# Optimization experiments

Hardware: AMD Instinct MI355X
Metric: run time of the kernel (lower is better)

## Reference

```python
import jax, jax.numpy as jnp
import numpy as np

B, T, H, V = 32, 256, 1024, 50257


def setup_inputs() -> dict:
    key = jax.random.key(0)
    k1, k2, k3, k4 = jax.random.split(key, 4)
    # log-normalized HMM parameters, matching torch.log_softmax in __init__
    alpha = jax.nn.log_softmax(jax.random.normal(k1, (H, H), dtype=jnp.float32), axis=1)
    beta = jax.nn.log_softmax(jax.random.normal(k2, (H, V), dtype=jnp.float32), axis=1)
    gamma = jax.nn.log_softmax(jax.random.normal(k3, (H,), dtype=jnp.float32), axis=0)
    x = jax.random.randint(k4, (B, T), 0, V)
    return {"x": x, "alpha": alpha, "beta": beta, "gamma": gamma}


def reference(x, alpha, beta, gamma):
    # emission log-probs gathered per token: e[b, t, h] = beta[h, x[b, t]]
    e = beta.T[x]  # [B, T, H]

    # backward-in-time recurrence:
    #   y_{T-1} = e[:, T-1]
    #   y_t     = logsumexp_j(alpha[i, j] + y_{t+1}[b, j]) + e[:, t]
    y0 = e[:, -1]  # [B, H]

    def step(y, e_t):
        y = jax.nn.logsumexp(alpha[None, :, :] + y[:, None, :], axis=2) + e_t
        return y, None

    # scan over t = T-2 .. 0 (reverse time order)
    es = jnp.flip(e[:, :-1], axis=1).transpose(1, 0, 2)  # [T-1, B, H]
    y, _ = jax.lax.scan(step, y0, es)

    # final marginalization over initial-state distribution gamma
    return jax.nn.logsumexp(gamma[None, :] + y, axis=1)  # [B]
```

## Files before the change

### kernel.cpp

```cpp
#include <hip/hip_runtime.h>
#include <hip/hip_bf16.h>


#define Hdim 1024
#define Bdim 32
#define Tdim 256
#define Vdim 50257
#define NWG  16
#define SLICE 64

typedef __attribute__((ext_vector_type(8))) __bf16 bf16x8;
typedef __attribute__((ext_vector_type(4))) float  f32x4;
typedef __attribute__((ext_vector_type(4))) unsigned u32x4;

#define OFF_ABF   0
#define OFF_YBUF  2097152
#define OFF_PSUM  (OFF_YBUF + 131072)
#define OFF_RBUF  (OFF_PSUM + 128)
#define OFF_WREC  (OFF_RBUF + 128)
#define OFF_FLG   (OFF_WREC + 8192)
#define OFF_END0  (OFF_FLG + 8192)
#define OFF_E     (((OFF_END0) + 4095) & ~4095)
#define WS_E_NEED ((size_t)OFF_E + (size_t)Tdim * Bdim * Hdim * 4)

#define SM_A       131072
#define SMEM_BYTES (SM_A + 256)

__device__ __forceinline__ void st_b128_sc(void* p, u32x4 v) {
    asm volatile("global_store_dwordx4 %0, %1, off sc0 sc1" :: "v"(p), "v"(v) : "memory");
}
__device__ __forceinline__ void st_b32_sc(void* p, unsigned v) {
    asm volatile("global_store_dword %0, %1, off sc0 sc1" :: "v"(p), "v"(v) : "memory");
}
__device__ __forceinline__ void st_b16_sc(void* p, unsigned v) {
    asm volatile("global_store_short %0, %1, off sc0 sc1" :: "v"(p), "v"(v) : "memory");
}
__device__ __forceinline__ u32x4 ld_b128_sc(const void* p) {
    u32x4 r;
    asm volatile("global_load_dwordx4 %0, %1, off sc0 sc1" : "=v"(r) : "v"(p) : "memory");
    return r;
}
__device__ __forceinline__ float ld_f32_sc(const void* p) {
    float r;
    asm volatile("global_load_dword %0, %1, off sc0 sc1" : "=v"(r) : "v"(p) : "memory");
    return r;
}
__device__ __forceinline__ unsigned ld_u32sync_sc(const void* p) {
    unsigned r;
    asm volatile("global_load_dword %0, %1, off sc0 sc1\n\ts_waitcnt vmcnt(0)"
                 : "=v"(r) : "v"(p) : "memory");
    return r;
}
__device__ __forceinline__ void waitcnt_vm0() {
    asm volatile("s_waitcnt vmcnt(0)" ::: "memory");
    __builtin_amdgcn_sched_barrier(0);
}
__device__ __forceinline__ void waitcnt_vm32() {
    asm volatile("s_waitcnt vmcnt(32)" ::: "memory");
    __builtin_amdgcn_sched_barrier(0);
}

__global__ void k_expA(const float* __restrict__ alpha, __bf16* __restrict__ Abf) {
    int idx = (blockIdx.x * 256 + threadIdx.x) * 4;
    float4 v = *(const float4*)(alpha + idx);
    union { __bf16 h[4]; uint2 u; } cv;
    cv.h[0] = (__bf16)__expf(v.x);
    cv.h[1] = (__bf16)__expf(v.y);
    cv.h[2] = (__bf16)__expf(v.z);
    cv.h[3] = (__bf16)__expf(v.w);
    *(uint2*)(Abf + idx) = cv.u;
}

__global__ void k_gather(const int* __restrict__ x, const float* __restrict__ beta,
                         float* __restrict__ E) {
    int tb = blockIdx.x;
    int t  = tb >> 5, b = tb & 31;
    int xv = x[b * Tdim + t];
    int i  = threadIdx.x * 4;
    float4 v;
    v.x = beta[(size_t)(i + 0) * Vdim + xv];
    v.y = beta[(size_t)(i + 1) * Vdim + xv];
    v.z = beta[(size_t)(i + 2) * Vdim + xv];
    v.w = beta[(size_t)(i + 3) * Vdim + xv];
    *(float4*)(E + ((size_t)t * Bdim + b) * Hdim + i) = v;
}

__device__ __forceinline__ void load_e(const float* __restrict__ E,
                                       const float* __restrict__ beta,
                                       const int* __restrict__ x,
                                       int t, int b0, int i0, int useE, float e[2][4]) {
    if (useE) {
        #pragma unroll
        for (int u = 0; u < 2; ++u)
            #pragma unroll
            for (int r = 0; r < 4; ++r)
                e[u][r] = E[((size_t)t * Bdim + (b0 + r)) * Hdim + i0 + u * 16];
    } else {
        int xv[4];
        #pragma unroll
        for (int r = 0; r < 4; ++r) xv[r] = x[(b0 + r) * Tdim + t];
        #pragma unroll
        for (int u = 0; u < 2; ++u)
            #pragma unroll
            for (int r = 0; r < 4; ++r)
                e[u][r] = beta[(size_t)(i0 + u * 16) * Vdim + xv[r]];
    }
}

__device__ __forceinline__ void publish_wave(const float y[2][4], const float Gc[4],
                                             char* Yblk,
                                             char* wrec_pw,
                                             char* flg_pw,
                                             int li, int g, int np, int b0,
                                             unsigned seq) {
    float mx[4];
    #pragma unroll
    for (int r = 0; r < 4; ++r) {
        #pragma unroll
        for (int u = 0; u < 2; ++u) {
            float Yn = __expf(y[u][r] - Gc[r]);
            __bf16 h = (__bf16)Yn;
            unsigned hv = (unsigned)__builtin_bit_cast(unsigned short, h);
            st_b16_sc(Yblk + (b0 + r) * 128 + (np * 32 + u * 16 + li) * 2, hv);
        }
        float m = fmaxf(y[0][r], y[1][r]);
        m = fmaxf(m, __shfl_xor(m, 1, 16));
        m = fmaxf(m, __shfl_xor(m, 2, 16));
        m = fmaxf(m, __shfl_xor(m, 4, 16));
        m = fmaxf(m, __shfl_xor(m, 8, 16));
        mx[r] = m;
    }
    if (li == 0) {
        f32x4 mv = {mx[0], mx[1], mx[2], mx[3]};
        st_b128_sc(wrec_pw + g * 16, __builtin_bit_cast(u32x4, mv));
    }
    asm volatile("s_waitcnt vmcnt(0)" ::: "memory");
    if ((threadIdx.x & 63) == 0) st_b32_sc(flg_pw, seq);
}

__launch_bounds__(256, 1)
__global__ void k_hmm(const int* __restrict__ x,
                      const float* __restrict__ beta,
                      const float* __restrict__ gamma,
                      const __bf16* __restrict__ Abf,
                      char* __restrict__ Yb,
                      char* __restrict__ wrec,
                      char* __restrict__ flg,
                      float* __restrict__ Psum,
                      float* __restrict__ Rbuf,
                      const float* __restrict__ Ebuf,
                      int useE)
{
    extern __shared__ char smem[];
    char* Asl = smem;

    const int p   = blockIdx.x;
    const int tid = threadIdx.x;
    const int w   = tid >> 6;
    const int l   = tid & 63;
    const int g   = l >> 4;
    const int li  = l & 15;
    const int mb  = w & 1;
    const int np  = w >> 1;
    const int b0  = mb * 16 + g * 4;
    const int i0  = p * SLICE + np * 32 + li;

    #pragma unroll
    for (int rep = 0; rep < 32; ++rep) {
        int flat = rep * 256 + tid;
        int row  = flat >> 7;
        int c16  = flat & 127;
        uint4 v = *(const uint4*)((const char*)Abf + (size_t)(p * 64 + row) * 2048 + c16 * 16);
        int off = (row * 2048 + c16 * 16) ^ ((row & 7) << 4);
        *(uint4*)(Asl + off) = v;
    }
    __syncthreads();

    {
        float y0[2][4];
        load_e(Ebuf, beta, x, Tdim - 1, b0, i0, useE, y0);
        float Gc0[4] = {0.f, 0.f, 0.f, 0.f};
        publish_wave(y0, Gc0, Yb + p * 4096,
                     wrec + (size_t)p * 256 + w * 64,
                     flg + (size_t)(p * 4 + w) * 64,
                     li, g, np, b0, 1u);
    }

    float Nprev[4] = {0.f, 0.f, 0.f, 0.f};
    float ereg[2][4];
    load_e(Ebuf, beta, x, Tdim - 2, b0, i0, useE, ereg);

    for (int s = 1; s < Tdim; ++s) {
        const int t     = Tdim - 1 - s;
        const int par_r = (s - 1) & 1;
        const int par_w = s & 1;

        float eregN[2][4];
        if (s < Tdim - 1) load_e(Ebuf, beta, x, t - 1, b0, i0, useE, eregN);
        float gl[2] = {0.f, 0.f};
        if (s == Tdim - 1) { gl[0] = gamma[i0]; gl[1] = gamma[i0 + 16]; }
        waitcnt_vm0();

        {
            const char* fp = flg + (size_t)par_r * 4096 + l * 64;
            while (!__all((int)(ld_u32sync_sc(fp) >= (unsigned)s))) {}
        }

        const char* Ybase = Yb + (size_t)par_r * (NWG * 4096);
        const char* yrow  = Ybase + (mb * 16 + li) * 128 + g * 16;
        u32x4 yreg[32];
        #pragma unroll
        for (int kc = 0; kc < 32; ++kc)
            yreg[kc] = ld_b128_sc(yrow + (kc >> 1) * 4096 + (kc & 1) * 64);

        float gmv[32];
        {
            const char* wbase = wrec + (size_t)par_r * 4096;
            if (l < 32) {
                int bmb = l >> 4;
                int idx = (l & 15) * 4;
                #pragma unroll
                for (int q = 0; q < 16; ++q) {
                    gmv[2 * q]     = ld_f32_sc(wbase + q * 256 + bmb * 64 + idx);
                    gmv[2 * q + 1] = ld_f32_sc(wbase + q * 256 + (bmb + 2) * 64 + idx);
                }
            }
        }

        waitcnt_vm32();

        f32x4 acc0 = {0.f, 0.f, 0.f, 0.f}, acc1 = {0.f, 0.f, 0.f, 0.f};
        {
            const int ia = np * 32 + li;
            const int ib = ia + 16;
            const int basea = ia * 2048 + g * 16, xa = (ia & 7) << 4;
            const int baseb = ib * 2048 + g * 16, xb = (ib & 7) << 4;
            #pragma unroll
            for (int kc = 0; kc < 32; ++kc) {
                bf16x8 af0 = *(const bf16x8*)(Asl + ((basea + kc * 64) ^ xa));
                bf16x8 af1 = *(const bf16x8*)(Asl + ((baseb + kc * 64) ^ xb));
                bf16x8 yf  = __builtin_bit_cast(bf16x8, yreg[kc]);
                acc0 = __builtin_amdgcn_mfma_f32_16x16x32_bf16(yf, af0, acc0, 0, 0, 0);
                acc1 = __builtin_amdgcn_mfma_f32_16x16x32_bf16(yf, af1, acc1, 0, 0, 0);
            }
        }

        waitcnt_vm0();

        float gm = -3.0e38f;
        if (l < 32) {
            #pragma unroll
            for (int q = 0; q < 32; ++q) gm = fmaxf(gm, gmv[q]);
        }
        float Gcur[4];
        #pragma unroll
        for (int r = 0; r < 4; ++r) Gcur[r] = __shfl(gm, b0 + r);

        float yv[2][4];
        #pragma unroll
        for (int r = 0; r < 4; ++r) {
            yv[0][r] = Nprev[r] + __logf(acc0[r]) + ereg[0][r];
            yv[1][r] = Nprev[r] + __logf(acc1[r]) + ereg[1][r];
        }

        if (s < Tdim - 1) {
            publish_wave(yv, Gcur,
                         Yb + (size_t)par_w * (NWG * 4096) + p * 4096,
                         wrec + (size_t)par_w * 4096 + (size_t)p * 256 + w * 64,
                         flg + (size_t)par_w * 4096 + (size_t)(p * 4 + w) * 64,
                         li, g, np, b0, (unsigned)(s + 1));
            #pragma unroll
            for (int r = 0; r < 4; ++r) Nprev[r] = Gcur[r];
            #pragma unroll
            for (int u = 0; u < 2; ++u)
                #pragma unroll
                for (int r = 0; r < 4; ++r) ereg[u][r] = eregN[u][r];
        } else {
            #pragma unroll
            for (int r = 0; r < 4; ++r) {
                float pa = __expf(gl[0] + yv[0][r] - Gcur[r])
                         + __expf(gl[1] + yv[1][r] - Gcur[r]);
                pa += __shfl_xor(pa, 1, 16);
                pa += __shfl_xor(pa, 2, 16);
                pa += __shfl_xor(pa, 4, 16);
                pa += __shfl_xor(pa, 8, 16);
                if (li == 0) {
                    atomicAdd(&Psum[b0 + r], pa);
                    if (p == 0) Rbuf[b0 + r] = Gcur[r];
                }
            }
        }
    }
}

__global__ void k_final(const float* __restrict__ Psum, const float* __restrict__ Rbuf,
                        float* __restrict__ out) {
    int b = threadIdx.x;
    if (b < 32) out[b] = Rbuf[b] + __logf(Psum[b]);
}

extern "C" void kernel_launch(void* const* d_in, const int* in_sizes, int n_in,
                              void* d_out, int out_size, void* d_ws, size_t ws_size,
                              hipStream_t stream) {
    const int*   x     = (const int*)d_in[0];
    const float* alpha = (const float*)d_in[1];
    const float* beta  = (const float*)d_in[2];
    const float* gamma = (const float*)d_in[3];

    char* ws = (char*)d_ws;
    __bf16* Abf  = (__bf16*)(ws + OFF_ABF);
    char*   Yb   = ws + OFF_YBUF;
    float*  Psum = (float*)(ws + OFF_PSUM);
    float*  Rbuf = (float*)(ws + OFF_RBUF);
    char*   wrec = ws + OFF_WREC;
    char*   flg  = ws + OFF_FLG;
    float*  Ebuf = (float*)(ws + OFF_E);

    int useE = (ws_size >= WS_E_NEED) ? 1 : 0;

    (void)hipMemsetAsync(ws + OFF_PSUM, 0, OFF_END0 - OFF_PSUM, stream);

    hipLaunchKernelGGL(k_expA, dim3((Hdim * Hdim) / (256 * 4)), dim3(256), 0, stream, alpha, Abf);

    if (useE)
        hipLaunchKernelGGL(k_gather, dim3(Tdim * Bdim), dim3(256), 0, stream, x, beta, Ebuf);

    (void)hipFuncSetAttribute((const void*)k_hmm, hipFuncAttributeMaxDynamicSharedMemorySize, SMEM_BYTES);
    hipLaunchKernelGGL(k_hmm, dim3(NWG), dim3(256), SMEM_BYTES, stream,
                       x, beta, gamma, Abf, Yb, wrec, flg, Psum, Rbuf,
                       useE ? Ebuf : (const float*)nullptr, useE);

    hipLaunchKernelGGL(k_final, dim3(1), dim3(64), 0, stream, Psum, Rbuf, (float*)d_out);
}
```

Baseline: 2.018 ms.

## Replace flag-based grid sync with sign-tagged data validity polling

Removes the separate per-wave flag stores and the flag spin-wait. Consumers now repeatedly load the Y buffer and the max records until every value carries the expected epoch tag. The tag is the bf16 sign bit, which flips every two steps via a negation factor, and the max records are paired with a step tag. Each step then needs one store-to-load round trip instead of two (data wait, then flag), at the cost of re-reading the full Y tile on every failed poll. The Y buffer is pre-filled so the initial sign pattern matches no valid epoch.

```diff
diff --git a/kernel.cpp b/kernel.cpp
--- a/kernel.cpp
+++ b/kernel.cpp
@@ -12,51 +12,38 @@
 typedef __attribute__((ext_vector_type(8))) __bf16 bf16x8;
 typedef __attribute__((ext_vector_type(4))) float  f32x4;
 typedef __attribute__((ext_vector_type(4))) unsigned u32x4;
+typedef __attribute__((ext_vector_type(2))) unsigned u32x2;
 
 #define OFF_ABF   0
 #define OFF_YBUF  2097152
 #define OFF_PSUM  (OFF_YBUF + 131072)
 #define OFF_RBUF  (OFF_PSUM + 128)
 #define OFF_WREC  (OFF_RBUF + 128)
-#define OFF_FLG   (OFF_WREC + 8192)
-#define OFF_END0  (OFF_FLG + 8192)
+#define OFF_END0  (OFF_WREC + 16384)
 #define OFF_E     (((OFF_END0) + 4095) & ~4095)
 #define WS_E_NEED ((size_t)OFF_E + (size_t)Tdim * Bdim * Hdim * 4)
 
 #define SM_A       131072
 #define SMEM_BYTES (SM_A + 256)
 
-__device__ __forceinline__ void st_b128_sc(void* p, u32x4 v) {
-    asm volatile("global_store_dwordx4 %0, %1, off sc0 sc1" :: "v"(p), "v"(v) : "memory");
-}
-__device__ __forceinline__ void st_b32_sc(void* p, unsigned v) {
-    asm volatile("global_store_dword %0, %1, off sc0 sc1" :: "v"(p), "v"(v) : "memory");
-}
 __device__ __forceinline__ void st_b16_sc(void* p, unsigned v) {
     asm volatile("global_store_short %0, %1, off sc0 sc1" :: "v"(p), "v"(v) : "memory");
+}
+__device__ __forceinline__ void st_b64_sc(void* p, u32x2 v) {
+    asm volatile("global_store_dwordx2 %0, %1, off sc0 sc1" :: "v"(p), "v"(v) : "memory");
 }
 __device__ __forceinline__ u32x4 ld_b128_sc(const void* p) {
     u32x4 r;
     asm volatile("global_load_dwordx4 %0, %1, off sc0 sc1" : "=v"(r) : "v"(p) : "memory");
     return r;
 }
-__device__ __forceinline__ float ld_f32_sc(const void* p) {
-    float r;
-    asm volatile("global_load_dword %0, %1, off sc0 sc1" : "=v"(r) : "v"(p) : "memory");
-    return r;
-}
-__device__ __forceinline__ unsigned ld_u32sync_sc(const void* p) {
-    unsigned r;
-    asm volatile("global_load_dword %0, %1, off sc0 sc1\n\ts_waitcnt vmcnt(0)"
-                 : "=v"(r) : "v"(p) : "memory");
+__device__ __forceinline__ u32x2 ld_b64_sc(const void* p) {
+    u32x2 r;
+    asm volatile("global_load_dwordx2 %0, %1, off sc0 sc1" : "=v"(r) : "v"(p) : "memory");
     return r;
 }
 __device__ __forceinline__ void waitcnt_vm0() {
     asm volatile("s_waitcnt vmcnt(0)" ::: "memory");
-    __builtin_amdgcn_sched_barrier(0);
-}
-__device__ __forceinline__ void waitcnt_vm32() {
-    asm volatile("s_waitcnt vmcnt(32)" ::: "memory");
     __builtin_amdgcn_sched_barrier(0);
 }
 
@@ -109,17 +96,16 @@
 
 __device__ __forceinline__ void publish_wave(const float y[2][4], const float Gc[4],
                                              char* Yblk,
-                                             char* wrec_pw,
-                                             char* flg_pw,
+                                             char* wrec_w,
                                              int li, int g, int np, int b0,
-                                             unsigned seq) {
+                                             unsigned tag, float wneg) {
     float mx[4];
     #pragma unroll
     for (int r = 0; r < 4; ++r) {
         #pragma unroll
         for (int u = 0; u < 2; ++u) {
             float Yn = __expf(y[u][r] - Gc[r]);
-            __bf16 h = (__bf16)Yn;
+            __bf16 h = (__bf16)(Yn * wneg);
             unsigned hv = (unsigned)__builtin_bit_cast(unsigned short, h);
             st_b16_sc(Yblk + (b0 + r) * 128 + (np * 32 + u * 16 + li) * 2, hv);
         }
@@ -131,11 +117,12 @@
         mx[r] = m;
     }
     if (li == 0) {
-        f32x4 mv = {mx[0], mx[1], mx[2], mx[3]};
-        st_b128_sc(wrec_pw + g * 16, __builtin_bit_cast(u32x4, mv));
-    }
-    asm volatile("s_waitcnt vmcnt(0)" ::: "memory");
-    if ((threadIdx.x & 63) == 0) st_b32_sc(flg_pw, seq);
+        #pragma unroll
+        for (int r = 0; r < 4; ++r) {
+            u32x2 pr = { __builtin_bit_cast(unsigned, mx[r]), tag };
+            st_b64_sc(wrec_w + g * 32 + r * 8, pr);
+        }
+    }
 }
 
 __launch_bounds__(256, 1)
@@ -145,7 +132,6 @@
                       const __bf16* __restrict__ Abf,
                       char* __restrict__ Yb,
                       char* __restrict__ wrec,
-                      char* __restrict__ flg,
                       float* __restrict__ Psum,
                       float* __restrict__ Rbuf,
                       const float* __restrict__ Ebuf,
@@ -165,6 +151,11 @@
     const int b0  = mb * 16 + g * 4;
     const int i0  = p * SLICE + np * 32 + li;
 
+    const int wl_bmb = (l >> 4) & 1;
+    const int wl_w   = wl_bmb + ((l >> 5) << 1);
+    const int wl_bi  = l & 15;
+    const int wl_off = wl_w * 128 + (wl_bi >> 2) * 32 + (wl_bi & 3) * 8;
+
     #pragma unroll
     for (int rep = 0; rep < 32; ++rep) {
         int flat = rep * 256 + tid;
@@ -181,9 +172,8 @@
         load_e(Ebuf, beta, x, Tdim - 1, b0, i0, useE, y0);
         float Gc0[4] = {0.f, 0.f, 0.f, 0.f};
         publish_wave(y0, Gc0, Yb + p * 4096,
-                     wrec + (size_t)p * 256 + w * 64,
-                     flg + (size_t)(p * 4 + w) * 64,
-                     li, g, np, b0, 1u);
+                     wrec + (size_t)p * 512 + w * 128,
+                     li, g, np, b0, 1u, 1.f);
     }
 
     float Nprev[4] = {0.f, 0.f, 0.f, 0.f};
@@ -194,40 +184,54 @@
         const int t     = Tdim - 1 - s;
         const int par_r = (s - 1) & 1;
         const int par_w = s & 1;
+        const unsigned want = (unsigned)s;
+        const unsigned sgnr = (((s - 1) >> 1) & 1) ? 0x80008000u : 0u;
+        const float    negr = (((s - 1) >> 1) & 1) ? -1.f : 1.f;
+        const float    negw = ((s >> 1) & 1) ? -1.f : 1.f;
 
         float eregN[2][4];
         if (s < Tdim - 1) load_e(Ebuf, beta, x, t - 1, b0, i0, useE, eregN);
         float gl[2] = {0.f, 0.f};
         if (s == Tdim - 1) { gl[0] = gamma[i0]; gl[1] = gamma[i0 + 16]; }
-        waitcnt_vm0();
-
-        {
-            const char* fp = flg + (size_t)par_r * 4096 + l * 64;
-            while (!__all((int)(ld_u32sync_sc(fp) >= (unsigned)s))) {}
-        }
 
         const char* Ybase = Yb + (size_t)par_r * (NWG * 4096);
         const char* yrow  = Ybase + (mb * 16 + li) * 128 + g * 16;
+        const char* wbase = wrec + (size_t)par_r * 8192 + wl_off;
+
         u32x4 yreg[32];
-        #pragma unroll
-        for (int kc = 0; kc < 32; ++kc)
-            yreg[kc] = ld_b128_sc(yrow + (kc >> 1) * 4096 + (kc & 1) * 64);
-
-        float gmv[32];
-        {
-            const char* wbase = wrec + (size_t)par_r * 4096;
-            if (l < 32) {
-                int bmb = l >> 4;
-                int idx = (l & 15) * 4;
-                #pragma unroll
-                for (int q = 0; q < 16; ++q) {
-                    gmv[2 * q]     = ld_f32_sc(wbase + q * 256 + bmb * 64 + idx);
-                    gmv[2 * q + 1] = ld_f32_sc(wbase + q * 256 + (bmb + 2) * 64 + idx);
-                }
+        u32x2 wr[16];
+        int okc;
+        do {
+            #pragma unroll
+            for (int kc = 0; kc < 32; ++kc)
+                yreg[kc] = ld_b128_sc(yrow + (kc >> 1) * 4096 + (kc & 1) * 64);
+            #pragma unroll
+            for (int q = 0; q < 16; ++q)
+                wr[q] = ld_b64_sc(wbase + q * 512);
+            waitcnt_vm0();
+            unsigned bad = 0;
+            #pragma unroll
+            for (int kc = 0; kc < 32; ++kc) {
+                bad |= (yreg[kc][0] ^ sgnr) & 0x80008000u;
+                bad |= (yreg[kc][1] ^ sgnr) & 0x80008000u;
+                bad |= (yreg[kc][2] ^ sgnr) & 0x80008000u;
+                bad |= (yreg[kc][3] ^ sgnr) & 0x80008000u;
             }
-        }
-
-        waitcnt_vm32();
+            #pragma unroll
+            for (int q = 0; q < 16; ++q)
+                bad |= (wr[q][1] ^ want);
+            okc = __all(bad == 0);
+        } while (!okc);
+
+        float gm = __builtin_bit_cast(float, wr[0][0]);
+        #pragma unroll
+        for (int q = 1; q < 16; ++q)
+            gm = fmaxf(gm, __builtin_bit_cast(float, wr[q][0]));
+        gm = fmaxf(gm, __shfl_xor(gm, 32));
+
+        float Gcur[4];
+        #pragma unroll
+        for (int r = 0; r < 4; ++r) Gcur[r] = __shfl(gm, mb * 16 + g * 4 + r);
 
         f32x4 acc0 = {0.f, 0.f, 0.f, 0.f}, acc1 = {0.f, 0.f, 0.f, 0.f};
         {
@@ -245,30 +249,18 @@
             }
         }
 
-        waitcnt_vm0();
-
-        float gm = -3.0e38f;
-        if (l < 32) {
-            #pragma unroll
-            for (int q = 0; q < 32; ++q) gm = fmaxf(gm, gmv[q]);
-        }
-        float Gcur[4];
-        #pragma unroll
-        for (int r = 0; r < 4; ++r) Gcur[r] = __shfl(gm, b0 + r);
-
         float yv[2][4];
         #pragma unroll
         for (int r = 0; r < 4; ++r) {
-            yv[0][r] = Nprev[r] + __logf(acc0[r]) + ereg[0][r];
-            yv[1][r] = Nprev[r] + __logf(acc1[r]) + ereg[1][r];
+            yv[0][r] = Nprev[r] + __logf(acc0[r] * negr) + ereg[0][r];
+            yv[1][r] = Nprev[r] + __logf(acc1[r] * negr) + ereg[1][r];
         }
 
         if (s < Tdim - 1) {
             publish_wave(yv, Gcur,
                          Yb + (size_t)par_w * (NWG * 4096) + p * 4096,
-                         wrec + (size_t)par_w * 4096 + (size_t)p * 256 + w * 64,
-                         flg + (size_t)par_w * 4096 + (size_t)(p * 4 + w) * 64,
-                         li, g, np, b0, (unsigned)(s + 1));
+                         wrec + (size_t)par_w * 8192 + (size_t)p * 512 + w * 128,
+                         li, g, np, b0, (unsigned)(s + 1), negw);
             #pragma unroll
             for (int r = 0; r < 4; ++r) Nprev[r] = Gcur[r];
             #pragma unroll
@@ -313,11 +305,11 @@
     float*  Psum = (float*)(ws + OFF_PSUM);
     float*  Rbuf = (float*)(ws + OFF_RBUF);
     char*   wrec = ws + OFF_WREC;
-    char*   flg  = ws + OFF_FLG;
     float*  Ebuf = (float*)(ws + OFF_E);
 
     int useE = (ws_size >= WS_E_NEED) ? 1 : 0;
 
+    (void)hipMemsetAsync(ws + OFF_YBUF, 0xAA, 131072, stream);
     (void)hipMemsetAsync(ws + OFF_PSUM, 0, OFF_END0 - OFF_PSUM, stream);
 
     hipLaunchKernelGGL(k_expA, dim3((Hdim * Hdim) / (256 * 4)), dim3(256), 0, stream, alpha, Abf);
@@ -327,7 +319,7 @@
 
     (void)hipFuncSetAttribute((const void*)k_hmm, hipFuncAttributeMaxDynamicSharedMemorySize, SMEM_BYTES);
     hipLaunchKernelGGL(k_hmm, dim3(NWG), dim3(256), SMEM_BYTES, stream,
-                       x, beta, gamma, Abf, Yb, wrec, flg, Psum, Rbuf,
+                       x, beta, gamma, Abf, Yb, wrec, Psum, Rbuf,
                        useE ? Ebuf : (const float*)nullptr, useE);
 
     hipLaunchKernelGGL(k_final, dim3(1), dim3(64), 0, stream, Psum, Rbuf, (float*)d_out);
```

Result: slower. 2.920 ms (+44.7%).

## Replace per-wave flag polling with atomic counters and overlap emission loads

Applied to the files above, without the earlier changes.

Each wave now publishes by atomically incrementing one shared per-parity counter, instead of writing its own sequence flag. Consumers spin on a single counter load rather than 64 flag loads combined with a wave-wide all-reduce. In the E-buffer path, the next step's emission loads are issued after the Y loads and use cached global loads, so they overlap with the MFMA work. A waitcnt of 8 keeps them outstanding. The kernel is templated on useE to drop the runtime branches, and the gamma load is hoisted out of the loop. The risk is contention on one atomic counter across 64 waves, plus the relaxed-ordering correctness of the counter handshake.

```diff
diff --git a/kernel.cpp b/kernel.cpp
--- a/kernel.cpp
+++ b/kernel.cpp
@@ -18,22 +18,23 @@
 #define OFF_PSUM  (OFF_YBUF + 131072)
 #define OFF_RBUF  (OFF_PSUM + 128)
 #define OFF_WREC  (OFF_RBUF + 128)
-#define OFF_FLG   (OFF_WREC + 8192)
-#define OFF_END0  (OFF_FLG + 8192)
+#define OFF_CNT   (OFF_WREC + 8192)
+#define OFF_END0  (OFF_CNT + 256)
 #define OFF_E     (((OFF_END0) + 4095) & ~4095)
 #define WS_E_NEED ((size_t)OFF_E + (size_t)Tdim * Bdim * Hdim * 4)
 
 #define SM_A       131072
 #define SMEM_BYTES (SM_A + 256)
 
+#define WAITCNT_VM(n) do { \
+    asm volatile("s_waitcnt vmcnt(" #n ")" ::: "memory"); \
+    __builtin_amdgcn_sched_barrier(0); } while (0)
+
+__device__ __forceinline__ void st_b16_sc(void* p, unsigned v) {
+    asm volatile("global_store_short %0, %1, off sc0 sc1" :: "v"(p), "v"(v) : "memory");
+}
 __device__ __forceinline__ void st_b128_sc(void* p, u32x4 v) {
     asm volatile("global_store_dwordx4 %0, %1, off sc0 sc1" :: "v"(p), "v"(v) : "memory");
-}
-__device__ __forceinline__ void st_b32_sc(void* p, unsigned v) {
-    asm volatile("global_store_dword %0, %1, off sc0 sc1" :: "v"(p), "v"(v) : "memory");
-}
-__device__ __forceinline__ void st_b16_sc(void* p, unsigned v) {
-    asm volatile("global_store_short %0, %1, off sc0 sc1" :: "v"(p), "v"(v) : "memory");
 }
 __device__ __forceinline__ u32x4 ld_b128_sc(const void* p) {
     u32x4 r;
@@ -45,19 +46,10 @@
     asm volatile("global_load_dword %0, %1, off sc0 sc1" : "=v"(r) : "v"(p) : "memory");
     return r;
 }
-__device__ __forceinline__ unsigned ld_u32sync_sc(const void* p) {
-    unsigned r;
-    asm volatile("global_load_dword %0, %1, off sc0 sc1\n\ts_waitcnt vmcnt(0)"
-                 : "=v"(r) : "v"(p) : "memory");
+__device__ __forceinline__ float ld_f32_cached(const void* p) {
+    float r;
+    asm volatile("global_load_dword %0, %1, off" : "=v"(r) : "v"(p) : "memory");
     return r;
-}
-__device__ __forceinline__ void waitcnt_vm0() {
-    asm volatile("s_waitcnt vmcnt(0)" ::: "memory");
-    __builtin_amdgcn_sched_barrier(0);
-}
-__device__ __forceinline__ void waitcnt_vm32() {
-    asm volatile("s_waitcnt vmcnt(32)" ::: "memory");
-    __builtin_amdgcn_sched_barrier(0);
 }
 
 __global__ void k_expA(const float* __restrict__ alpha, __bf16* __restrict__ Abf) {
@@ -110,9 +102,8 @@
 __device__ __forceinline__ void publish_wave(const float y[2][4], const float Gc[4],
                                              char* Yblk,
                                              char* wrec_pw,
-                                             char* flg_pw,
-                                             int li, int g, int np, int b0,
-                                             unsigned seq) {
+                                             unsigned* cnt_w,
+                                             int l, int li, int g, int np, int b0) {
     float mx[4];
     #pragma unroll
     for (int r = 0; r < 4; ++r) {
@@ -134,10 +125,12 @@
         f32x4 mv = {mx[0], mx[1], mx[2], mx[3]};
         st_b128_sc(wrec_pw + g * 16, __builtin_bit_cast(u32x4, mv));
     }
-    asm volatile("s_waitcnt vmcnt(0)" ::: "memory");
-    if ((threadIdx.x & 63) == 0) st_b32_sc(flg_pw, seq);
-}
-
+    WAITCNT_VM(0);
+    if (l == 0)
+        __hip_atomic_fetch_add(cnt_w, 1u, __ATOMIC_RELAXED, __HIP_MEMORY_SCOPE_AGENT);
+}
+
+template<int USEE>
 __launch_bounds__(256, 1)
 __global__ void k_hmm(const int* __restrict__ x,
                       const float* __restrict__ beta,
@@ -145,11 +138,10 @@
                       const __bf16* __restrict__ Abf,
                       char* __restrict__ Yb,
                       char* __restrict__ wrec,
-                      char* __restrict__ flg,
+                      unsigned* __restrict__ cnt,
                       float* __restrict__ Psum,
                       float* __restrict__ Rbuf,
-                      const float* __restrict__ Ebuf,
-                      int useE)
+                      const float* __restrict__ Ebuf)
 {
     extern __shared__ char smem[];
     char* Asl = smem;
@@ -176,34 +168,48 @@
     }
     __syncthreads();
 
+    const float gl0 = gamma[i0];
+    const float gl1 = gamma[i0 + 16];
+
     {
         float y0[2][4];
-        load_e(Ebuf, beta, x, Tdim - 1, b0, i0, useE, y0);
+        load_e(Ebuf, beta, x, Tdim - 1, b0, i0, USEE, y0);
         float Gc0[4] = {0.f, 0.f, 0.f, 0.f};
         publish_wave(y0, Gc0, Yb + p * 4096,
                      wrec + (size_t)p * 256 + w * 64,
-                     flg + (size_t)(p * 4 + w) * 64,
-                     li, g, np, b0, 1u);
+                     cnt, l, li, g, np, b0);
     }
 
     float Nprev[4] = {0.f, 0.f, 0.f, 0.f};
     float ereg[2][4];
-    load_e(Ebuf, beta, x, Tdim - 2, b0, i0, useE, ereg);
+    float eregN[2][4];
+
+    if constexpr (USEE) {
+        const float* Et = Ebuf + (size_t)(Tdim - 2) * (Bdim * Hdim);
+        #pragma unroll
+        for (int u = 0; u < 2; ++u)
+            #pragma unroll
+            for (int r = 0; r < 4; ++r)
+                ereg[u][r] = ld_f32_cached(Et + (b0 + r) * Hdim + i0 + u * 16);
+        WAITCNT_VM(0);
+    } else {
+        load_e(Ebuf, beta, x, Tdim - 2, b0, i0, 0, ereg);
+    }
 
     for (int s = 1; s < Tdim; ++s) {
         const int t     = Tdim - 1 - s;
         const int par_r = (s - 1) & 1;
         const int par_w = s & 1;
 
-        float eregN[2][4];
-        if (s < Tdim - 1) load_e(Ebuf, beta, x, t - 1, b0, i0, useE, eregN);
-        float gl[2] = {0.f, 0.f};
-        if (s == Tdim - 1) { gl[0] = gamma[i0]; gl[1] = gamma[i0 + 16]; }
-        waitcnt_vm0();
+        if constexpr (!USEE) {
+            if (s < Tdim - 1) load_e(Ebuf, beta, x, t - 1, b0, i0, 0, eregN);
+            WAITCNT_VM(0);
+        }
 
         {
-            const char* fp = flg + (size_t)par_r * 4096 + l * 64;
-            while (!__all((int)(ld_u32sync_sc(fp) >= (unsigned)s))) {}
+            const unsigned tgt = 64u * (((unsigned)s + 1u) >> 1);
+            unsigned* cp = cnt + (size_t)par_r * 32;
+            while (__hip_atomic_load(cp, __ATOMIC_RELAXED, __HIP_MEMORY_SCOPE_AGENT) < tgt) {}
         }
 
         const char* Ybase = Yb + (size_t)par_r * (NWG * 4096);
@@ -227,7 +233,18 @@
             }
         }
 
-        waitcnt_vm32();
+        if constexpr (USEE) {
+            const int tE = (t > 0) ? (t - 1) : 0;
+            const float* Et = Ebuf + (size_t)tE * (Bdim * Hdim);
+            #pragma unroll
+            for (int u = 0; u < 2; ++u)
+                #pragma unroll
+                for (int r = 0; r < 4; ++r)
+                    eregN[u][r] = ld_f32_cached(Et + (b0 + r) * Hdim + i0 + u * 16);
+            WAITCNT_VM(8);
+        } else {
+            WAITCNT_VM(0);
+        }
 
         f32x4 acc0 = {0.f, 0.f, 0.f, 0.f}, acc1 = {0.f, 0.f, 0.f, 0.f};
         {
@@ -245,8 +262,6 @@
             }
         }
 
-        waitcnt_vm0();
-
         float gm = -3.0e38f;
         if (l < 32) {
             #pragma unroll
@@ -267,8 +282,8 @@
             publish_wave(yv, Gcur,
                          Yb + (size_t)par_w * (NWG * 4096) + p * 4096,
                          wrec + (size_t)par_w * 4096 + (size_t)p * 256 + w * 64,
-                         flg + (size_t)par_w * 4096 + (size_t)(p * 4 + w) * 64,
-                         li, g, np, b0, (unsigned)(s + 1));
+                         cnt + (size_t)par_w * 32,
+                         l, li, g, np, b0);
             #pragma unroll
             for (int r = 0; r < 4; ++r) Nprev[r] = Gcur[r];
             #pragma unroll
@@ -278,8 +293,8 @@
         } else {
             #pragma unroll
             for (int r = 0; r < 4; ++r) {
-                float pa = __expf(gl[0] + yv[0][r] - Gcur[r])
-                         + __expf(gl[1] + yv[1][r] - Gcur[r]);
+                float pa = __expf(gl0 + yv[0][r] - Gcur[r])
+                         + __expf(gl1 + yv[1][r] - Gcur[r]);
                 pa += __shfl_xor(pa, 1, 16);
                 pa += __shfl_xor(pa, 2, 16);
                 pa += __shfl_xor(pa, 4, 16);
@@ -308,13 +323,13 @@
     const float* gamma = (const float*)d_in[3];
 
     char* ws = (char*)d_ws;
-    __bf16* Abf  = (__bf16*)(ws + OFF_ABF);
-    char*   Yb   = ws + OFF_YBUF;
-    float*  Psum = (float*)(ws + OFF_PSUM);
-    float*  Rbuf = (float*)(ws + OFF_RBUF);
-    char*   wrec = ws + OFF_WREC;
-    char*   flg  = ws + OFF_FLG;
-    float*  Ebuf = (float*)(ws + OFF_E);
+    __bf16*   Abf  = (__bf16*)(ws + OFF_ABF);
+    char*     Yb   = ws + OFF_YBUF;
+    float*    Psum = (float*)(ws + OFF_PSUM);
+    float*    Rbuf = (float*)(ws + OFF_RBUF);
+    char*     wrec = ws + OFF_WREC;
+    unsigned* cnt  = (unsigned*)(ws + OFF_CNT);
+    float*    Ebuf = (float*)(ws + OFF_E);
 
     int useE = (ws_size >= WS_E_NEED) ? 1 : 0;
 
@@ -322,13 +337,16 @@
 
     hipLaunchKernelGGL(k_expA, dim3((Hdim * Hdim) / (256 * 4)), dim3(256), 0, stream, alpha, Abf);
 
-    if (useE)
+    if (useE) {
         hipLaunchKernelGGL(k_gather, dim3(Tdim * Bdim), dim3(256), 0, stream, x, beta, Ebuf);
-
-    (void)hipFuncSetAttribute((const void*)k_hmm, hipFuncAttributeMaxDynamicSharedMemorySize, SMEM_BYTES);
-    hipLaunchKernelGGL(k_hmm, dim3(NWG), dim3(256), SMEM_BYTES, stream,
-                       x, beta, gamma, Abf, Yb, wrec, flg, Psum, Rbuf,
-                       useE ? Ebuf : (const float*)nullptr, useE);
+        (void)hipFuncSetAttribute((const void*)k_hmm<1>, hipFuncAttributeMaxDynamicSharedMemorySize, SMEM_BYTES);
+        hipLaunchKernelGGL(k_hmm<1>, dim3(NWG), dim3(256), SMEM_BYTES, stream,
+                           x, beta, gamma, Abf, Yb, wrec, cnt, Psum, Rbuf, Ebuf);
+    } else {
+        (void)hipFuncSetAttribute((const void*)k_hmm<0>, hipFuncAttributeMaxDynamicSharedMemorySize, SMEM_BYTES);
+        hipLaunchKernelGGL(k_hmm<0>, dim3(NWG), dim3(256), SMEM_BYTES, stream,
+                           x, beta, gamma, Abf, Yb, wrec, cnt, Psum, Rbuf, (const float*)nullptr);
+    }
 
     hipLaunchKernelGGL(k_final, dim3(1), dim3(64), 0, stream, Psum, Rbuf, (float*)d_out);
 }
```

Measured after the change: 2.341 ms. 16.0% more time.

## Fuse emission gather into recurrence kernel as extra blocks with per-timestep ready flags

Applied to the files above, without the earlier changes.

Removes the separate gather kernel. The gather work now runs as extra blocks of the recurrence launch, in reverse time order, so it overlaps with the sequential HMM recurrence. Each timestep's gather blocks bump an atomic ready counter, and recurrence blocks poll it before loading the emissions they need. Once a global counter shows all gathers are done, polling stops. The cost is polling latency inside the serial loop, and the gather blocks inherit the large dynamic LDS allocation, which may limit how many run concurrently.

```diff
diff --git a/kernel.cpp b/kernel.cpp
--- a/kernel.cpp
+++ b/kernel.cpp
@@ -8,6 +8,7 @@
 #define Vdim 50257
 #define NWG  16
 #define SLICE 64
+#define NGATHER (Tdim * Bdim)
 
 typedef __attribute__((ext_vector_type(8))) __bf16 bf16x8;
 typedef __attribute__((ext_vector_type(4))) float  f32x4;
@@ -19,21 +20,23 @@
 #define OFF_RBUF  (OFF_PSUM + 128)
 #define OFF_WREC  (OFF_RBUF + 128)
 #define OFF_FLG   (OFF_WREC + 8192)
-#define OFF_END0  (OFF_FLG + 8192)
+#define OFF_ERDY  (OFF_FLG + 8192)
+#define OFF_GRD   (OFF_ERDY + 16384)
+#define OFF_END0  (OFF_GRD + 128)
 #define OFF_E     (((OFF_END0) + 4095) & ~4095)
 #define WS_E_NEED ((size_t)OFF_E + (size_t)Tdim * Bdim * Hdim * 4)
 
 #define SM_A       131072
 #define SMEM_BYTES (SM_A + 256)
 
+__device__ __forceinline__ void st_b16_sc(void* p, unsigned v) {
+    asm volatile("global_store_short %0, %1, off sc0 sc1" :: "v"(p), "v"(v) : "memory");
+}
+__device__ __forceinline__ void st_b32_sc(void* p, unsigned v) {
+    asm volatile("global_store_dword %0, %1, off sc0 sc1" :: "v"(p), "v"(v) : "memory");
+}
 __device__ __forceinline__ void st_b128_sc(void* p, u32x4 v) {
     asm volatile("global_store_dwordx4 %0, %1, off sc0 sc1" :: "v"(p), "v"(v) : "memory");
-}
-__device__ __forceinline__ void st_b32_sc(void* p, unsigned v) {
-    asm volatile("global_store_dword %0, %1, off sc0 sc1" :: "v"(p), "v"(v) : "memory");
-}
-__device__ __forceinline__ void st_b16_sc(void* p, unsigned v) {
-    asm volatile("global_store_short %0, %1, off sc0 sc1" :: "v"(p), "v"(v) : "memory");
 }
 __device__ __forceinline__ u32x4 ld_b128_sc(const void* p) {
     u32x4 r;
@@ -71,20 +74,6 @@
     *(uint2*)(Abf + idx) = cv.u;
 }
 
-__global__ void k_gather(const int* __restrict__ x, const float* __restrict__ beta,
-                         float* __restrict__ E) {
-    int tb = blockIdx.x;
-    int t  = tb >> 5, b = tb & 31;
-    int xv = x[b * Tdim + t];
-    int i  = threadIdx.x * 4;
-    float4 v;
-    v.x = beta[(size_t)(i + 0) * Vdim + xv];
-    v.y = beta[(size_t)(i + 1) * Vdim + xv];
-    v.z = beta[(size_t)(i + 2) * Vdim + xv];
-    v.w = beta[(size_t)(i + 3) * Vdim + xv];
-    *(float4*)(E + ((size_t)t * Bdim + b) * Hdim + i) = v;
-}
-
 __device__ __forceinline__ void load_e(const float* __restrict__ E,
                                        const float* __restrict__ beta,
                                        const int* __restrict__ x,
@@ -138,6 +127,15 @@
     if ((threadIdx.x & 63) == 0) st_b32_sc(flg_pw, seq);
 }
 
+__device__ __forceinline__ void poll_eready(const char* erdy, const char* grd,
+                                            int t, int* edone) {
+    if (*edone) return;
+    if (ld_u32sync_sc(grd) >= (unsigned)NGATHER) { *edone = 1; return; }
+    const char* ep = erdy + (size_t)t * 64;
+    while (ld_u32sync_sc(ep) < (unsigned)Bdim) {}
+}
+
+template<int USEE>
 __launch_bounds__(256, 1)
 __global__ void k_hmm(const int* __restrict__ x,
                       const float* __restrict__ beta,
@@ -146,11 +144,34 @@
                       char* __restrict__ Yb,
                       char* __restrict__ wrec,
                       char* __restrict__ flg,
+                      char* __restrict__ erdy,
+                      char* __restrict__ grd,
                       float* __restrict__ Psum,
                       float* __restrict__ Rbuf,
-                      const float* __restrict__ Ebuf,
-                      int useE)
+                      float* __restrict__ Ebuf)
 {
+    if (USEE && blockIdx.x >= NWG) {
+        const int idx = blockIdx.x - NWG;
+        const int t   = (Tdim - 1) - (idx >> 5);
+        const int b   = idx & 31;
+        const int xv  = x[b * Tdim + t];
+        const int i   = threadIdx.x * 4;
+        f32x4 v;
+        v[0] = beta[(size_t)(i + 0) * Vdim + xv];
+        v[1] = beta[(size_t)(i + 1) * Vdim + xv];
+        v[2] = beta[(size_t)(i + 2) * Vdim + xv];
+        v[3] = beta[(size_t)(i + 3) * Vdim + xv];
+        st_b128_sc(Ebuf + ((size_t)t * Bdim + b) * Hdim + i,
+                   __builtin_bit_cast(u32x4, v));
+        waitcnt_vm0();
+        __syncthreads();
+        if (threadIdx.x == 0) {
+            atomicAdd((unsigned*)(erdy + (size_t)t * 64), 1u);
+            atomicAdd((unsigned*)grd, 1u);
+        }
+        return;
+    }
+
     extern __shared__ char smem[];
     char* Asl = smem;
 
@@ -165,6 +186,8 @@
     const int b0  = mb * 16 + g * 4;
     const int i0  = p * SLICE + np * 32 + li;
 
+    int edone = USEE ? 0 : 1;
+
     #pragma unroll
     for (int rep = 0; rep < 32; ++rep) {
         int flat = rep * 256 + tid;
@@ -176,9 +199,11 @@
     }
     __syncthreads();
 
+    poll_eready(erdy, grd, Tdim - 1, &edone);
+    poll_eready(erdy, grd, Tdim - 2, &edone);
     {
         float y0[2][4];
-        load_e(Ebuf, beta, x, Tdim - 1, b0, i0, useE, y0);
+        load_e(Ebuf, beta, x, Tdim - 1, b0, i0, USEE, y0);
         float Gc0[4] = {0.f, 0.f, 0.f, 0.f};
         publish_wave(y0, Gc0, Yb + p * 4096,
                      wrec + (size_t)p * 256 + w * 64,
@@ -188,7 +213,7 @@
 
     float Nprev[4] = {0.f, 0.f, 0.f, 0.f};
     float ereg[2][4];
-    load_e(Ebuf, beta, x, Tdim - 2, b0, i0, useE, ereg);
+    load_e(Ebuf, beta, x, Tdim - 2, b0, i0, USEE, ereg);
 
     for (int s = 1; s < Tdim; ++s) {
         const int t     = Tdim - 1 - s;
@@ -196,7 +221,10 @@
         const int par_w = s & 1;
 
         float eregN[2][4];
-        if (s < Tdim - 1) load_e(Ebuf, beta, x, t - 1, b0, i0, useE, eregN);
+        if (s < Tdim - 1) {
+            poll_eready(erdy, grd, t - 1, &edone);
+            load_e(Ebuf, beta, x, t - 1, b0, i0, USEE, eregN);
+        }
         float gl[2] = {0.f, 0.f};
         if (s == Tdim - 1) { gl[0] = gamma[i0]; gl[1] = gamma[i0 + 16]; }
         waitcnt_vm0();
@@ -314,6 +342,8 @@
     float*  Rbuf = (float*)(ws + OFF_RBUF);
     char*   wrec = ws + OFF_WREC;
     char*   flg  = ws + OFF_FLG;
+    char*   erdy = ws + OFF_ERDY;
+    char*   grd  = ws + OFF_GRD;
     float*  Ebuf = (float*)(ws + OFF_E);
 
     int useE = (ws_size >= WS_E_NEED) ? 1 : 0;
@@ -322,13 +352,15 @@
 
     hipLaunchKernelGGL(k_expA, dim3((Hdim * Hdim) / (256 * 4)), dim3(256), 0, stream, alpha, Abf);
 
-    if (useE)
-        hipLaunchKernelGGL(k_gather, dim3(Tdim * Bdim), dim3(256), 0, stream, x, beta, Ebuf);
-
-    (void)hipFuncSetAttribute((const void*)k_hmm, hipFuncAttributeMaxDynamicSharedMemorySize, SMEM_BYTES);
-    hipLaunchKernelGGL(k_hmm, dim3(NWG), dim3(256), SMEM_BYTES, stream,
-                       x, beta, gamma, Abf, Yb, wrec, flg, Psum, Rbuf,
-                       useE ? Ebuf : (const float*)nullptr, useE);
+    if (useE) {
+        (void)hipFuncSetAttribute((const void*)k_hmm<1>, hipFuncAttributeMaxDynamicSharedMemorySize, SMEM_BYTES);
+        hipLaunchKernelGGL(k_hmm<1>, dim3(NWG + NGATHER), dim3(256), SMEM_BYTES, stream,
+                           x, beta, gamma, Abf, Yb, wrec, flg, erdy, grd, Psum, Rbuf, Ebuf);
+    } else {
+        (void)hipFuncSetAttribute((const void*)k_hmm<0>, hipFuncAttributeMaxDynamicSharedMemorySize, SMEM_BYTES);
+        hipLaunchKernelGGL(k_hmm<0>, dim3(NWG), dim3(256), SMEM_BYTES, stream,
+                           x, beta, gamma, Abf, Yb, wrec, flg, erdy, grd, Psum, Rbuf, (float*)nullptr);
+    }
 
     hipLaunchKernelGGL(k_final, dim3(1), dim3(64), 0, stream, Psum, Rbuf, (float*)d_out);
 }
```

After: 1.966 ms. 2.6% less time.
